# Performance work log

Measured on AMD Instinct MI355X. Metric: run time of the kernel, lower is better.

Reference implementation:

```python
import jax, jax.numpy as jnp
import numpy as np

H = 12          # num_attention_heads
D = 64          # attention_head_size
HID = H * D     # hidden_size = 768
M = 1024        # max_position_embeddings


def setup_inputs() -> dict:
    key = jax.random.key(0)
    ks = jax.random.split(key, 9)
    B, S = 4, 1024
    s = 0.02
    return {
        "hidden_states": jax.random.normal(ks[0], (B, S, HID), jnp.float32),
        "attention_mask": jnp.zeros((B, 1, 1, S), jnp.float32),
        "Wq": jax.random.normal(ks[1], (HID, HID), jnp.float32) * s,
        "bq": jnp.zeros((HID,), jnp.float32),
        "Wk": jax.random.normal(ks[2], (HID, HID), jnp.float32) * s,
        "bk": jnp.zeros((HID,), jnp.float32),
        "Wv": jax.random.normal(ks[3], (HID, HID), jnp.float32) * s,
        "bv": jnp.zeros((HID,), jnp.float32),
        "dist_emb": jax.random.normal(ks[4], (2 * M - 1, D), jnp.float32) * s,
    }


def reference(hidden_states, attention_mask, Wq, bq, Wk, bk, Wv, bv, dist_emb):
    B, S, _ = hidden_states.shape

    def heads(x):  # [B,S,HID] -> [B,H,S,D]
        return x.reshape(B, S, H, D).transpose(0, 2, 1, 3)

    q = heads(hidden_states @ Wq + bq)
    k = heads(hidden_states @ Wk + bk)
    v = heads(hidden_states @ Wv + bv)

    # raw dot-product scores [B,H,S,S]
    scores = jnp.einsum('bhld,bhrd->bhlr', q, k)

    # relative_key_query positional bias
    pos = jnp.arange(S)
    distance = pos[:, None] - pos[None, :] + (M - 1)   # [S,S] in [0, 2M-2]
    pe = dist_emb[distance]                            # [S,S,D]
    scores = scores + jnp.einsum('bhld,lrd->bhlr', q, pe) \
                    + jnp.einsum('bhrd,lrd->bhlr', k, pe)

    scores = scores / jnp.sqrt(jnp.asarray(D, scores.dtype)) + attention_mask
    probs = jax.nn.softmax(scores, axis=-1)            # dropout is identity in eval

    ctx = jnp.einsum('bhlr,bhrd->bhld', probs, v)      # [B,H,S,D]
    ctx = ctx.transpose(0, 2, 1, 3).reshape(B, S, HID)
    return ctx, probs
```

## Files before the change

### kernel.cpp

```cpp
#include <hip/hip_runtime.h>
#include <hip/hip_bf16.h>

#define DEVFN __device__ __forceinline__

typedef __bf16 bf16x8 __attribute__((ext_vector_type(8)));
typedef float f32x4 __attribute__((ext_vector_type(4)));
typedef unsigned short ushort8 __attribute__((ext_vector_type(8)));
typedef unsigned short us4 __attribute__((ext_vector_type(4)));

namespace {

constexpr int S = 1024;
constexpr int HID = 768;
constexpr int NH = 12;
constexpr int HD = 64;

DEVFN unsigned short f2bf(float f) {
  union { float f; unsigned u; } v; v.f = f;
  unsigned r = v.u + 0x7FFF + ((v.u >> 16) & 1);
  return (unsigned short)(r >> 16);
}

DEVFN float bf2f(unsigned short u) {
  union { unsigned u; float f; } v; v.u = ((unsigned)u) << 16; return v.f;
}

DEVFN f32x4 zero4() { return f32x4{0.f, 0.f, 0.f, 0.f}; }

DEVFN f32x4 mfma_bf16(bf16x8 a, bf16x8 b, f32x4 c) {
  return __builtin_amdgcn_mfma_f32_16x16x32_bf16(a, b, c, 0, 0, 0);
}

DEVFN void gload16(void* lds_base, const void* gsrc) {
  __builtin_amdgcn_global_load_lds(
      (const __attribute__((address_space(1))) void*)gsrc,
      (__attribute__((address_space(3))) void*)lds_base, 16, 0, 0);
}

DEVFN bf16x8 frag_ld(const char* tile, int row, int ch) {
  int chs = ch ^ (row & 7);
  return *(const bf16x8*)(tile + row * 128 + chs * 16);
}

__global__ void k0_cvt_x(const float* __restrict__ x, unsigned short* __restrict__ xb) {
  size_t i = (size_t)(blockIdx.x * 256 + threadIdx.x) * 8;
  float4 a = *(const float4*)(x + i);
  float4 c = *(const float4*)(x + i + 4);
  ushort8 o;
  o[0] = f2bf(a.x); o[1] = f2bf(a.y); o[2] = f2bf(a.z); o[3] = f2bf(a.w);
  o[4] = f2bf(c.x); o[5] = f2bf(c.y); o[6] = f2bf(c.z); o[7] = f2bf(c.w);
  *(ushort8*)(xb + i) = o;
}

__global__ void k0_cvt_pe(const float* __restrict__ de, unsigned short* __restrict__ peb) {
  size_t i = (size_t)(blockIdx.x * 256 + threadIdx.x) * 8;
  int row = (int)(i >> 6);
  ushort8 o;
  if (row < 2047) {
    float4 a = *(const float4*)(de + i);
    float4 c = *(const float4*)(de + i + 4);
    o[0] = f2bf(a.x); o[1] = f2bf(a.y); o[2] = f2bf(a.z); o[3] = f2bf(a.w);
    o[4] = f2bf(c.x); o[5] = f2bf(c.y); o[6] = f2bf(c.z); o[7] = f2bf(c.w);
  } else {
    o = ushort8{0, 0, 0, 0, 0, 0, 0, 0};
  }
  *(ushort8*)(peb + i) = o;
}

__global__ __launch_bounds__(256) void k0_wt(const float* __restrict__ Wq,
                                             const float* __restrict__ Wk,
                                             const float* __restrict__ Wv,
                                             unsigned short* __restrict__ wt) {
  __shared__ float t[64][65];
  int bidx = blockIdx.x;
  int sec = bidx / 144, rem = bidx % 144;
  int ktb = rem / 12, ntb = rem % 12;
  const float* W = (sec == 0) ? Wq : ((sec == 1) ? Wk : Wv);
  int k0 = ktb * 64, n0 = ntb * 64;
  int tid = threadIdx.x;
  #pragma unroll
  for (int p = 0; p < 4; ++p) {
    int id = p * 256 + tid;
    int row = id >> 4, ch = id & 15;
    float4 v = *(const float4*)(W + (size_t)(k0 + row) * 768 + n0 + ch * 4);
    t[row][ch * 4 + 0] = v.x; t[row][ch * 4 + 1] = v.y;
    t[row][ch * 4 + 2] = v.z; t[row][ch * 4 + 3] = v.w;
  }
  __syncthreads();
  #pragma unroll
  for (int p = 0; p < 2; ++p) {
    int id = p * 256 + tid;
    int nrow = id >> 3, c8 = id & 7;
    ushort8 o;
    #pragma unroll
    for (int i = 0; i < 8; ++i) o[i] = f2bf(t[c8 * 8 + i][nrow]);
    *(ushort8*)(wt + (size_t)(sec * 768 + n0 + nrow) * 768 + k0 + c8 * 8) = o;
  }
}

__global__ __launch_bounds__(256) void k1_qkv(
    const unsigned short* __restrict__ xb, const unsigned short* __restrict__ wt,
    const float* __restrict__ bq, const float* __restrict__ bk, const float* __restrict__ bv,
    unsigned short* __restrict__ q_ws, unsigned short* __restrict__ k_ws,
    unsigned short* __restrict__ vt_ws) {
  __shared__ char ldsA[8192], ldsB[8192];
  const int tid = threadIdx.x, lane = tid & 63, wv = tid >> 6;
  const int row16 = lane & 15, cgrp = lane >> 4;
  const int ntb = blockIdx.x % 36, mtb = blockIdx.x / 36;
  const int sec = ntb / 12;
  const int n0 = ntb * 64;
  const int m0 = mtb * 64;

  f32x4 acc[4] = {zero4(), zero4(), zero4(), zero4()};

  for (int k0 = 0; k0 < 768; k0 += 64) {
    #pragma unroll
    for (int c = 0; c < 2; ++c) {
      int cc = (wv * 2 + c) * 64 + lane;
      int row = cc >> 3, ch = cc & 7, chs = ch ^ (row & 7);
      gload16(ldsA + (wv * 2 + c) * 1024, xb + (size_t)(m0 + row) * 768 + k0 + chs * 8);
      gload16(ldsB + (wv * 2 + c) * 1024, wt + (size_t)(n0 + row) * 768 + k0 + chs * 8);
    }
    __syncthreads();
    if (sec < 2) {
      bf16x8 af[2];
      #pragma unroll
      for (int k2 = 0; k2 < 2; ++k2) af[k2] = frag_ld(ldsA, wv * 16 + row16, k2 * 4 + cgrp);
      #pragma unroll
      for (int nt = 0; nt < 4; ++nt)
        #pragma unroll
        for (int k2 = 0; k2 < 2; ++k2) {
          bf16x8 bf = frag_ld(ldsB, nt * 16 + row16, k2 * 4 + cgrp);
          acc[nt] = mfma_bf16(af[k2], bf, acc[nt]);
        }
    } else {
      bf16x8 af[2];
      #pragma unroll
      for (int k2 = 0; k2 < 2; ++k2) af[k2] = frag_ld(ldsB, wv * 16 + row16, k2 * 4 + cgrp);
      #pragma unroll
      for (int mt = 0; mt < 4; ++mt)
        #pragma unroll
        for (int k2 = 0; k2 < 2; ++k2) {
          bf16x8 bx = frag_ld(ldsA, mt * 16 + row16, k2 * 4 + cgrp);
          acc[mt] = mfma_bf16(af[k2], bx, acc[mt]);
        }
    }
    __syncthreads();
  }

  if (sec < 2) {
    unsigned short* dst = (sec == 0) ? q_ws : k_ws;
    const float* bias = (sec == 0) ? bq : bk;
    int nl0 = (ntb % 12) * 64;
    #pragma unroll
    for (int nt = 0; nt < 4; ++nt) {
      int nn = nl0 + nt * 16 + row16;
      float bb = bias[nn];
      int hh = nn >> 6, dd = nn & 63;
      #pragma unroll
      for (int j = 0; j < 4; ++j) {
        int m = m0 + wv * 16 + cgrp * 4 + j;
        int b_ = m >> 10, s_ = m & 1023;
        dst[(size_t)((b_ * 12 + hh) * 1024 + s_) * 64 + dd] = f2bf(acc[nt][j] + bb);
      }
    }
  } else {
    int nl0 = (ntb % 12) * 64;
    #pragma unroll
    for (int j = 0; j < 4; ++j) {
      int nn = nl0 + wv * 16 + cgrp * 4 + j;
      float bb = bv[nn];
      int hh = nn >> 6, dd = nn & 63;
      #pragma unroll
      for (int mt = 0; mt < 4; ++mt) {
        int m = m0 + mt * 16 + row16;
        int b_ = m >> 10, s_ = m & 1023;
        vt_ws[(size_t)((b_ * 12 + hh) * 64 + dd) * 1024 + s_] = f2bf(acc[mt][j] + bb);
      }
    }
  }
}

__global__ __launch_bounds__(256) void k2_score(
    const unsigned short* __restrict__ q_ws, const unsigned short* __restrict__ k_ws,
    const unsigned short* __restrict__ peb, const float* __restrict__ mask,
    unsigned short* __restrict__ p_out, float* __restrict__ rsum_part) {
  __shared__ __align__(16) char kpe_lds[24576];
  __shared__ unsigned short p_sh[64 * 64];
  __shared__ float rsum_sh[2][64];

  char* k_lds = kpe_lds;
  char* pe_lds = kpe_lds + 8192;

  const int tid = threadIdx.x, lane = tid & 63, wv = tid >> 6;
  const int wl = wv >> 1, wr = wv & 1;
  const int row16 = lane & 15, cgrp = lane >> 4;

  const int bid = blockIdx.x;
  const int swz = (bid & 7) * 1536 + (bid >> 3);
  const int rt = swz & 15, lt = (swz >> 4) & 15, bh = swz >> 8;
  const int b = bh / NH;
  const int l0 = lt * 64, r0 = rt * 64;

  const unsigned short* qh = q_ws + (size_t)bh * S * HD;
  const unsigned short* khp = k_ws + (size_t)bh * S * HD;
  const float* maskb = mask + b * S;

  #pragma unroll
  for (int c = 0; c < 2; ++c) {
    int cc = (wv * 2 + c) * 64 + lane;
    int row = cc >> 3, ch = cc & 7, chs = ch ^ (row & 7);
    gload16(k_lds + (wv * 2 + c) * 1024, khp + (size_t)(r0 + row) * HD + chs * 8);
  }
  {
    int m0 = l0 - r0 + 960;
    #pragma unroll
    for (int c = 0; c < 4; ++c) {
      int cc = (wv * 4 + c) * 64 + lane;
      int row = cc >> 3, ch = cc & 7, chs = ch ^ (row & 7);
      gload16(pe_lds + (wv * 4 + c) * 1024, peb + (size_t)(m0 + row) * HD + chs * 8);
    }
  }

  bf16x8 qf[2][2];
  #pragma unroll
  for (int ltl = 0; ltl < 2; ++ltl)
    #pragma unroll
    for (int k2 = 0; k2 < 2; ++k2)
      qf[ltl][k2] = *(const bf16x8*)(qh + (size_t)(l0 + wl * 32 + ltl * 16 + row16) * HD +
                                     k2 * 32 + cgrp * 8);
  __syncthreads();

  bf16x8 kf[2][2], pef[4][2];
  #pragma unroll
  for (int rtl = 0; rtl < 2; ++rtl)
    #pragma unroll
    for (int k2 = 0; k2 < 2; ++k2)
      kf[rtl][k2] = frag_ld(k_lds, wr * 32 + rtl * 16 + row16, k2 * 4 + cgrp);
  const int qb = (wl - wr) * 32 + 32;
  #pragma unroll
  for (int jt = 0; jt < 4; ++jt)
    #pragma unroll
    for (int k2 = 0; k2 < 2; ++k2)
      pef[jt][k2] = frag_ld(pe_lds, qb + jt * 16 + row16, k2 * 4 + cgrp);
  __syncthreads();

  unsigned short* s3w = (unsigned short*)kpe_lds + wv * (64 * 36);

  #pragma unroll
  for (int rtl = 0; rtl < 2; ++rtl)
    #pragma unroll
    for (int jt = 0; jt < 4; ++jt) {
      f32x4 a3 = zero4();
      a3 = mfma_bf16(kf[rtl][0], pef[jt][0], a3);
      a3 = mfma_bf16(kf[rtl][1], pef[jt][1], a3);
      us4 o;
      o[0] = f2bf(a3[0]); o[1] = f2bf(a3[1]); o[2] = f2bf(a3[2]); o[3] = f2bf(a3[3]);
      *(us4*)(s3w + (jt * 16 + row16) * 36 + rtl * 16 + cgrp * 4) = o;
    }

  f32x4 s1[2][2];
  #pragma unroll
  for (int ltl = 0; ltl < 2; ++ltl)
    #pragma unroll
    for (int rtl = 0; rtl < 2; ++rtl) {
      f32x4 a1 = zero4();
      a1 = mfma_bf16(qf[ltl][0], kf[rtl][0], a1);
      a1 = mfma_bf16(qf[ltl][1], kf[rtl][1], a1);
      s1[ltl][rtl] = a1;
    }
  f32x4 s2[2][4];
  #pragma unroll
  for (int ltl = 0; ltl < 2; ++ltl)
    #pragma unroll
    for (int jt = 0; jt < 4; ++jt) {
      f32x4 a2 = zero4();
      a2 = mfma_bf16(qf[ltl][0], pef[jt][0], a2);
      a2 = mfma_bf16(qf[ltl][1], pef[jt][1], a2);
      s2[ltl][jt] = a2;
    }

  float rs[2][4] = {};
  #pragma unroll
  for (int rtl = 0; rtl < 2; ++rtl) {
    float mval = maskb[r0 + wr * 32 + rtl * 16 + row16];
    #pragma unroll
    for (int ltl = 0; ltl < 2; ++ltl) {
      const int jtA = ltl - rtl + 1;
      #pragma unroll
      for (int j = 0; j < 4; ++j) {
        int dl = ltl * 16 + cgrp * 4 + j;
        int dr = rtl * 16 + row16;
        int jjq = dl - dr + 31;
        int src = (lane & 48) | (jjq & 15);
        float vA = __shfl(s2[ltl][jtA][j], src, 64);
        float vB = __shfl(s2[ltl][jtA + 1][j], src, 64);
        float b1 = ((jjq >> 4) == jtA) ? vA : vB;
        float b2 = bf2f(s3w[jjq * 36 + dr]);
        float logit = (s1[ltl][rtl][j] + b1 + b2) * 0.125f + mval;
        float p = __expf(logit);
        rs[ltl][j] += p;
        int dlb = wl * 32 + dl, drb = wr * 32 + dr;
        p_sh[dlb * 64 + (drb ^ ((dlb & 7) << 3))] = f2bf(p);
      }
    }
  }

  #pragma unroll
  for (int ltl = 0; ltl < 2; ++ltl)
    #pragma unroll
    for (int j = 0; j < 4; ++j) {
      float v = rs[ltl][j];
      v += __shfl_xor(v, 1, 64);
      v += __shfl_xor(v, 2, 64);
      v += __shfl_xor(v, 4, 64);
      v += __shfl_xor(v, 8, 64);
      rs[ltl][j] = v;
    }
  if (row16 == 0) {
    #pragma unroll
    for (int ltl = 0; ltl < 2; ++ltl)
      #pragma unroll
      for (int j = 0; j < 4; ++j)
        rsum_sh[wr][wl * 32 + ltl * 16 + cgrp * 4 + j] = rs[ltl][j];
  }
  __syncthreads();

  if (tid < 64)
    rsum_part[((size_t)(bh * 16 + lt) * 64 + tid) * 16 + rt] =
        rsum_sh[0][tid] + rsum_sh[1][tid];

  #pragma unroll
  for (int p2 = 0; p2 < 2; ++p2) {
    int id = p2 * 256 + tid, dl = id >> 3, c = id & 7;
    uint4 w = *(const uint4*)((const char*)p_sh + dl * 128 + (c ^ (dl & 7)) * 16);
    *(uint4*)(p_out + ((size_t)bh * S + l0 + dl) * S + r0 + c * 8) = w;
  }
}

__global__ __launch_bounds__(256) void k3_pv(
    const unsigned short* __restrict__ p_in, const unsigned short* __restrict__ vt_ws,
    const float* __restrict__ rsum_part, float* __restrict__ ctx_part,
    float* __restrict__ inv_ws, float* __restrict__ out_probs) {
  __shared__ char p_sh[2][8192];
  __shared__ float inv_sh[64];

  const int tid = threadIdx.x, lane = tid & 63, wv = tid >> 6;
  const int row16 = lane & 15, cgrp = lane >> 4;
  const int bid = blockIdx.x;
  const int swz = (bid & 7) * 384 + (bid >> 3);
  const int rq = swz & 3, lt = (swz >> 2) & 15, bh = swz >> 6;
  const int l0 = lt * 64, rbase = rq * 256;

  const unsigned short* vth = vt_ws + (size_t)bh * HD * S;
  float* probs_bh = out_probs + (size_t)bh * S * S;

  if (tid < 64) {
    const float4* pp =
        (const float4*)(rsum_part + ((size_t)(bh * 16 + lt) * 64 + tid) * 16);
    float s = 0.f;
    #pragma unroll
    for (int i = 0; i < 4; ++i) {
      float4 v = pp[i];
      s += v.x + v.y + v.z + v.w;
    }
    float iv = 1.0f / s;
    inv_sh[tid] = iv;
    if (rq == 0) inv_ws[bh * S + l0 + tid] = iv;
  }

  auto stage = [&](char* buf, int r0) {
    #pragma unroll
    for (int c = 0; c < 2; ++c) {
      int cc = (wv * 2 + c) * 64 + lane;
      int row = cc >> 3, ch = cc & 7, chs = ch ^ (row & 7);
      gload16(buf + (wv * 2 + c) * 1024,
              p_in + ((size_t)bh * S + l0 + row) * S + r0 + chs * 8);
    }
  };

  stage(p_sh[0], rbase);
  __syncthreads();

  f32x4 ctxacc[4] = {zero4(), zero4(), zero4(), zero4()};

  for (int it = 0; it < 4; ++it) {
    const int r0 = rbase + it * 64, cur = it & 1;
    if (it < 3) stage(p_sh[cur ^ 1], r0 + 64);
    const char* cb = p_sh[cur];

    #pragma unroll
    for (int p2 = 0; p2 < 2; ++p2) {
      int id = p2 * 256 + tid, dl = id >> 3, c = id & 7;
      uint4 w = *(const uint4*)(cb + dl * 128 + (c ^ (dl & 7)) * 16);
      const unsigned short* pu = (const unsigned short*)&w;
      float iv = inv_sh[dl];
      float* dst = probs_bh + (size_t)(l0 + dl) * S + r0 + c * 8;
      float4 lo{bf2f(pu[0]) * iv, bf2f(pu[1]) * iv, bf2f(pu[2]) * iv, bf2f(pu[3]) * iv};
      float4 hi{bf2f(pu[4]) * iv, bf2f(pu[5]) * iv, bf2f(pu[6]) * iv, bf2f(pu[7]) * iv};
      *(float4*)dst = lo; *(float4*)(dst + 4) = hi;
    }

    {
      int lrow = wv * 16 + row16;
      bf16x8 pa[2];
      #pragma unroll
      for (int kc = 0; kc < 2; ++kc) {
        int ch = kc * 4 + cgrp, chs = ch ^ (lrow & 7);
        pa[kc] = *(const bf16x8*)(cb + lrow * 128 + chs * 16);
      }
      #pragma unroll
      for (int dt = 0; dt < 4; ++dt) {
        bf16x8 vb0 = *(const bf16x8*)(vth + (size_t)(dt * 16 + row16) * S + r0 + cgrp * 8);
        bf16x8 vb1 = *(const bf16x8*)(vth + (size_t)(dt * 16 + row16) * S + r0 + 32 + cgrp * 8);
        ctxacc[dt] = mfma_bf16(pa[0], vb0, ctxacc[dt]);
        ctxacc[dt] = mfma_bf16(pa[1], vb1, ctxacc[dt]);
      }
    }
    __syncthreads();
  }

  #pragma unroll
  for (int dt = 0; dt < 4; ++dt)
    #pragma unroll
    for (int j = 0; j < 4; ++j) {
      int lr = wv * 16 + cgrp * 4 + j;
      ctx_part[((size_t)(rq * 48 + bh) * S + l0 + lr) * 64 + dt * 16 + row16] =
          ctxacc[dt][j];
    }
}

__global__ __launch_bounds__(256) void k4_red(
    const float* __restrict__ ctx_part, const float* __restrict__ inv_ws,
    float* __restrict__ out_ctx) {
  int gid = blockIdx.x * 256 + threadIdx.x;
  int t = gid >> 3, d0 = (gid & 7) * 8;
  int bh = t >> 10, l = t & 1023;
  float4 s0{0.f, 0.f, 0.f, 0.f}, s1{0.f, 0.f, 0.f, 0.f};
  #pragma unroll
  for (int rq = 0; rq < 4; ++rq) {
    const float* p = ctx_part + ((size_t)(rq * 48 + bh) * S + l) * 64 + d0;
    float4 a = *(const float4*)p;
    float4 b = *(const float4*)(p + 4);
    s0.x += a.x; s0.y += a.y; s0.z += a.z; s0.w += a.w;
    s1.x += b.x; s1.y += b.y; s1.z += b.z; s1.w += b.w;
  }
  float iv = inv_ws[t];
  s0.x *= iv; s0.y *= iv; s0.z *= iv; s0.w *= iv;
  s1.x *= iv; s1.y *= iv; s1.z *= iv; s1.w *= iv;
  int b_ = bh / NH, h = bh % NH;
  float* dst = out_ctx + ((size_t)(b_ * S + l)) * HID + h * HD + d0;
  *(float4*)dst = s0;
  *(float4*)(dst + 4) = s1;
}

}

extern "C" void kernel_launch(void* const* d_in, const int* in_sizes, int n_in,
                              void* d_out, int out_size, void* d_ws, size_t ws_size,
                              hipStream_t stream) {
  const float* hidden = (const float*)d_in[0];
  const float* mask   = (const float*)d_in[1];
  const float* Wq = (const float*)d_in[2];
  const float* bq = (const float*)d_in[3];
  const float* Wk = (const float*)d_in[4];
  const float* bk = (const float*)d_in[5];
  const float* Wv = (const float*)d_in[6];
  const float* bv = (const float*)d_in[7];
  const float* de = (const float*)d_in[8];

  unsigned short* ws = (unsigned short*)d_ws;
  unsigned short* q_ws  = ws;
  unsigned short* k_ws  = ws + 3145728;
  unsigned short* vt_ws = ws + 6291456;
  unsigned short* xb    = ws + 9437184;
  unsigned short* wt    = ws + 12582912;
  unsigned short* peb   = ws + 14352384;
  float* rsum_part = (float*)(ws + 14483456);
  unsigned short* p_ws  = ws + 16056320;
  float* ctx_part = (float*)(ws + 66387968);
  float* inv_ws   = (float*)(ws + 91553792);

  float* outc = (float*)d_out;
  float* outp = outc + (size_t)4 * 1024 * 768;

  hipLaunchKernelGGL(k0_cvt_x, dim3(1536), dim3(256), 0, stream, hidden, xb);
  hipLaunchKernelGGL(k0_cvt_pe, dim3(64), dim3(256), 0, stream, de, peb);
  hipLaunchKernelGGL(k0_wt, dim3(432), dim3(256), 0, stream, Wq, Wk, Wv, wt);
  hipLaunchKernelGGL(k1_qkv, dim3(2304), dim3(256), 0, stream,
                     xb, wt, bq, bk, bv, q_ws, k_ws, vt_ws);
  hipLaunchKernelGGL(k2_score, dim3(12288), dim3(256), 0, stream,
                     q_ws, k_ws, peb, mask, p_ws, rsum_part);
  hipLaunchKernelGGL(k3_pv, dim3(3072), dim3(256), 0, stream,
                     p_ws, vt_ws, rsum_part, ctx_part, inv_ws, outp);
  hipLaunchKernelGGL(k4_red, dim3(1536), dim3(256), 0, stream,
                     ctx_part, inv_ws, outc);
}
```

Baseline: 230.2 us.

## Drop split-K in PV kernel and fuse context reduction and normalization

The PV kernel no longer splits the key dimension into four quarters. Each block now loops over all 16 key tiles, scales its accumulator by the inverse row sum, and writes the final context directly, so the separate reduction kernel and the partial-context workspace are gone. This removes a kernel launch and the global write and read of the partial sums. In exchange the grid shrinks from 3072 to 768 blocks, each with a four-times-longer serial loop, which may lower occupancy and parallelism on a device with many CUs.

```diff
diff --git a/kernel.cpp b/kernel.cpp
--- a/kernel.cpp
+++ b/kernel.cpp
@@ -340,17 +340,18 @@
 
 __global__ __launch_bounds__(256) void k3_pv(
     const unsigned short* __restrict__ p_in, const unsigned short* __restrict__ vt_ws,
-    const float* __restrict__ rsum_part, float* __restrict__ ctx_part,
-    float* __restrict__ inv_ws, float* __restrict__ out_probs) {
+    const float* __restrict__ rsum_part, float* __restrict__ out_ctx,
+    float* __restrict__ out_probs) {
   __shared__ char p_sh[2][8192];
   __shared__ float inv_sh[64];
 
   const int tid = threadIdx.x, lane = tid & 63, wv = tid >> 6;
   const int row16 = lane & 15, cgrp = lane >> 4;
   const int bid = blockIdx.x;
-  const int swz = (bid & 7) * 384 + (bid >> 3);
-  const int rq = swz & 3, lt = (swz >> 2) & 15, bh = swz >> 6;
-  const int l0 = lt * 64, rbase = rq * 256;
+  const int swz = (bid & 7) * 96 + (bid >> 3);
+  const int lt = swz & 15, bh = swz >> 4;
+  const int b = bh / NH, h = bh % NH;
+  const int l0 = lt * 64;
 
   const unsigned short* vth = vt_ws + (size_t)bh * HD * S;
   float* probs_bh = out_probs + (size_t)bh * S * S;
@@ -364,9 +365,7 @@
       float4 v = pp[i];
       s += v.x + v.y + v.z + v.w;
     }
-    float iv = 1.0f / s;
-    inv_sh[tid] = iv;
-    if (rq == 0) inv_ws[bh * S + l0 + tid] = iv;
+    inv_sh[tid] = 1.0f / s;
   }
 
   auto stage = [&](char* buf, int r0) {
@@ -379,14 +378,14 @@
     }
   };
 
-  stage(p_sh[0], rbase);
+  stage(p_sh[0], 0);
   __syncthreads();
 
   f32x4 ctxacc[4] = {zero4(), zero4(), zero4(), zero4()};
 
-  for (int it = 0; it < 4; ++it) {
-    const int r0 = rbase + it * 64, cur = it & 1;
-    if (it < 3) stage(p_sh[cur ^ 1], r0 + 64);
+  for (int rt = 0; rt < 16; ++rt) {
+    const int r0 = rt * 64, cur = rt & 1;
+    if (rt < 15) stage(p_sh[cur ^ 1], r0 + 64);
     const char* cb = p_sh[cur];
 
     #pragma unroll
@@ -425,33 +424,9 @@
     #pragma unroll
     for (int j = 0; j < 4; ++j) {
       int lr = wv * 16 + cgrp * 4 + j;
-      ctx_part[((size_t)(rq * 48 + bh) * S + l0 + lr) * 64 + dt * 16 + row16] =
-          ctxacc[dt][j];
-    }
-}
-
-__global__ __launch_bounds__(256) void k4_red(
-    const float* __restrict__ ctx_part, const float* __restrict__ inv_ws,
-    float* __restrict__ out_ctx) {
-  int gid = blockIdx.x * 256 + threadIdx.x;
-  int t = gid >> 3, d0 = (gid & 7) * 8;
-  int bh = t >> 10, l = t & 1023;
-  float4 s0{0.f, 0.f, 0.f, 0.f}, s1{0.f, 0.f, 0.f, 0.f};
-  #pragma unroll
-  for (int rq = 0; rq < 4; ++rq) {
-    const float* p = ctx_part + ((size_t)(rq * 48 + bh) * S + l) * 64 + d0;
-    float4 a = *(const float4*)p;
-    float4 b = *(const float4*)(p + 4);
-    s0.x += a.x; s0.y += a.y; s0.z += a.z; s0.w += a.w;
-    s1.x += b.x; s1.y += b.y; s1.z += b.z; s1.w += b.w;
-  }
-  float iv = inv_ws[t];
-  s0.x *= iv; s0.y *= iv; s0.z *= iv; s0.w *= iv;
-  s1.x *= iv; s1.y *= iv; s1.z *= iv; s1.w *= iv;
-  int b_ = bh / NH, h = bh % NH;
-  float* dst = out_ctx + ((size_t)(b_ * S + l)) * HID + h * HD + d0;
-  *(float4*)dst = s0;
-  *(float4*)(dst + 4) = s1;
+      out_ctx[((size_t)(b * S + l0 + lr)) * HID + h * HD + dt * 16 + row16] =
+          ctxacc[dt][j] * inv_sh[lr];
+    }
 }
 
 }
@@ -478,8 +453,6 @@
   unsigned short* peb   = ws + 14352384;
   float* rsum_part = (float*)(ws + 14483456);
   unsigned short* p_ws  = ws + 16056320;
-  float* ctx_part = (float*)(ws + 66387968);
-  float* inv_ws   = (float*)(ws + 91553792);
 
   float* outc = (float*)d_out;
   float* outp = outc + (size_t)4 * 1024 * 768;
@@ -491,8 +464,6 @@
                      xb, wt, bq, bk, bv, q_ws, k_ws, vt_ws);
   hipLaunchKernelGGL(k2_score, dim3(12288), dim3(256), 0, stream,
                      q_ws, k_ws, peb, mask, p_ws, rsum_part);
-  hipLaunchKernelGGL(k3_pv, dim3(3072), dim3(256), 0, stream,
-                     p_ws, vt_ws, rsum_part, ctx_part, inv_ws, outp);
-  hipLaunchKernelGGL(k4_red, dim3(1536), dim3(256), 0, stream,
-                     ctx_part, inv_ws, outc);
-}
+  hipLaunchKernelGGL(k3_pv, dim3(768), dim3(256), 0, stream,
+                     p_ws, vt_ws, rsum_part, outc, outp);
+}
```

After: 206.7 us. -10.2%, faster.
